# Optimization experiments

Measured on AMD Instinct MI355X. Metric: run time of the kernel, lower is better.

## Reference

```python
import jax, jax.numpy as jnp
import numpy as np

D_EMBED, D_K, D_V = 1024, 64, 64
B, S = 4, 4096


def setup_inputs() -> dict:
    key = jax.random.key(0)
    k1, k2, k3, k4 = jax.random.split(key, 4)
    x = jax.random.normal(k1, (B, S, D_EMBED), dtype=jnp.float32)
    # nn.Linear(d_embed, d) stores weight as [d, d_embed]
    Wq = jax.random.normal(k2, (D_K, D_EMBED), dtype=jnp.float32) * (D_EMBED ** -0.5)
    Wk = jax.random.normal(k3, (D_K, D_EMBED), dtype=jnp.float32) * (D_EMBED ** -0.5)
    Wv = jax.random.normal(k4, (D_V, D_EMBED), dtype=jnp.float32) * (D_EMBED ** -0.5)
    return {"x": x, "Wq": Wq, "Wk": Wk, "Wv": Wv}


def reference(x, Wq, Wk, Wv):
    # self-attention: y = z = x
    key = jnp.einsum('bse,ke->bsk', x, Wk)
    query = jnp.einsum('bse,ke->bsk', x, Wq)
    value = jnp.einsum('bse,ve->bsv', x, Wv)
    d_k = key.shape[-1]
    weight = jnp.einsum('bqk,bsk->bqs', query, key) / (d_k ** 0.5)
    # Faithful to torch: tril then masked_fill(weight == 0, -inf)
    weight = jnp.tril(weight)
    weight = jnp.where(weight == 0, -jnp.inf, weight)
    weight = jax.nn.softmax(weight, axis=-1)
    return jnp.einsum('bqs,bsv->bqv', weight, value)
```

## Files before the change

### kernel.cpp

```cpp
#include <hip/hip_runtime.h>
#include <hip/hip_bf16.h>


typedef short s16x8 __attribute__((ext_vector_type(8)));
typedef float f32x4 __attribute__((ext_vector_type(4)));
typedef float f32x16 __attribute__((ext_vector_type(16)));
typedef unsigned u32x2 __attribute__((ext_vector_type(2)));

#define MFMA16(a, b, c) __builtin_amdgcn_mfma_f32_16x16x32_bf16(a, b, c, 0, 0, 0)
#define MFMA32(a, b, c) __builtin_amdgcn_mfma_f32_32x32x16_bf16(a, b, c, 0, 0, 0)

constexpr int SEQ = 4096;
constexpr int DE  = 1024;

__device__ __forceinline__ short f2bf(float f) {
    union { float f; unsigned u; } v; v.f = f;
    unsigned r = (v.u + 0x7FFFu + ((v.u >> 16) & 1u)) >> 16;
    return (short)r;
}
__device__ __forceinline__ unsigned fbits(float f) { union { float f; unsigned u; } v; v.f = f; return v.u; }
__device__ __forceinline__ float bitsf(unsigned u) { union { unsigned u; float f; } v; v.u = u; return v.f; }
__device__ __forceinline__ unsigned pk2(float a, float b) {
    return (fbits(b) & 0xFFFF0000u) | (fbits(a) >> 16);
}

#define GLDS(gp, lp)                                                          \
    __builtin_amdgcn_global_load_lds(                                         \
        (const __attribute__((address_space(1))) unsigned int*)(gp),          \
        (__attribute__((address_space(3))) unsigned int*)(lp), 16, 0, 0)

__global__ __launch_bounds__(256) void k_convw(const float* __restrict__ Wq,
                                               const float* __restrict__ Wk,
                                               const float* __restrict__ Wv,
                                               short* __restrict__ Wb) {
    int i = (blockIdx.x * 256 + threadIdx.x) * 4;
    if (i >= 192 * 1024) return;
    int n = i >> 10, k = i & 1023;
    const float* src; float sc;
    if (n < 64)       { src = Wq + n * 1024;         sc = 0.18033688011112042f; }
    else if (n < 128) { src = Wk + (n - 64) * 1024;  sc = 1.0f; }
    else              { src = Wv + (n - 128) * 1024; sc = 1.0f; }
    float4 v = *(const float4*)(src + k);
    short4 o;
    o.x = f2bf(v.x * sc); o.y = f2bf(v.y * sc);
    o.z = f2bf(v.z * sc); o.w = f2bf(v.w * sc);
    *(short4*)(Wb + i) = o;
}

__global__ __launch_bounds__(512) void k_proj(const float* __restrict__ x,
                                              const short* __restrict__ Wb,
                                              short* __restrict__ Qs,
                                              short* __restrict__ Ks,
                                              short* __restrict__ Vt) {
    __shared__ __align__(16) char lds[2][40960];
    const int tid  = threadIdx.x;
    const int lane = tid & 63;
    const int c = lane & 15, g = (lane >> 4) & 3;
    const int wv = tid >> 6;
    const int rg = wv & 3, nh = wv >> 2;
    const int n0 = nh * 96;
    const int m0 = blockIdx.x * 64;

    const int Ar  = tid >> 4;
    const int Acs = ((tid & 15) << 4) ^ ((Ar & 7) << 4);
    const char* aS0 = (const char*)x + (((size_t)(m0 + Ar)) << 12) + Acs;
    const char* aS1 = aS0 + ((size_t)32 << 12);
    const int Wr  = tid >> 3;
    const int Wcs = ((tid & 7) << 4) ^ ((Wr & 7) << 4);
    const char* wS0 = (const char*)Wb + (((size_t)Wr) << 11) + Wcs;
    const char* wS1 = wS0 + ((size_t)64 << 11);
    const char* wS2 = wS0 + ((size_t)128 << 11);

    char* db0 = &lds[0][0] + tid * 16;
    char* db1 = &lds[1][0] + tid * 16;

    const int arow = rg * 16 + c;
    const int swz  = (c & 7) << 4;
    const char* aR[2] = { &lds[0][0] + arow * 256, &lds[1][0] + arow * 256 };
    const char* wR[2][6];
#pragma unroll
    for (int nf = 0; nf < 6; nf++) {
        int wrow = n0 + nf * 16 + c;
        wR[0][nf] = &lds[0][0] + 16384 + wrow * 128;
        wR[1][nf] = &lds[1][0] + 16384 + wrow * 128;
    }

    f32x4 acc[6];
#pragma unroll
    for (int i = 0; i < 6; i++) acc[i] = (f32x4){0.f, 0.f, 0.f, 0.f};

#define PSTAGE(kk, db) {                                  \
        GLDS(aS0 + (kk) * 256, (db));                     \
        GLDS(aS1 + (kk) * 256, (db) + 8192);              \
        GLDS(wS0 + (kk) * 128, (db) + 16384);             \
        GLDS(wS1 + (kk) * 128, (db) + 24576);             \
        GLDS(wS2 + (kk) * 128, (db) + 32768); }

#define PCOMPUTE(bi) {                                                         \
        _Pragma("unroll")                                                      \
        for (int kc = 0; kc < 2; kc++) {                                       \
            float4 a0 = *(const float4*)(aR[bi] + ((kc*128 + g*32)      ^ swz)); \
            float4 a1 = *(const float4*)(aR[bi] + ((kc*128 + g*32 + 16) ^ swz)); \
            s16x8 a;                                                           \
            a[0]=f2bf(a0.x); a[1]=f2bf(a0.y); a[2]=f2bf(a0.z); a[3]=f2bf(a0.w); \
            a[4]=f2bf(a1.x); a[5]=f2bf(a1.y); a[6]=f2bf(a1.z); a[7]=f2bf(a1.w); \
            _Pragma("unroll")                                                  \
            for (int nf = 0; nf < 6; nf++) {                                   \
                s16x8 bfr = *(const s16x8*)(wR[bi][nf] + ((kc*64 + g*16) ^ swz)); \
                acc[nf] = MFMA16(a, bfr, acc[nf]);                             \
            }                                                                  \
        } }

    PSTAGE(0, db0);
    PSTAGE(1, db1);

    for (int kk = 0; kk < 15; kk++) {
        asm volatile("s_waitcnt vmcnt(5)" ::: "memory");
        __builtin_amdgcn_sched_barrier(0);
        __builtin_amdgcn_s_barrier();
        if (kk & 1) PCOMPUTE(1) else PCOMPUTE(0)
        asm volatile("s_waitcnt lgkmcnt(0)" ::: "memory");
        __builtin_amdgcn_sched_barrier(0);
        __builtin_amdgcn_s_barrier();
        if (kk < 14) { if (kk & 1) PSTAGE(kk + 2, db1) else PSTAGE(kk + 2, db0) }
    }
    asm volatile("s_waitcnt vmcnt(0)" ::: "memory");
    __builtin_amdgcn_sched_barrier(0);
    __builtin_amdgcn_s_barrier();
    PCOMPUTE(1)
#undef PSTAGE
#undef PCOMPUTE

#pragma unroll
    for (int nf = 0; nf < 6; nf++) {
        int col16 = n0 + nf * 16;
        if (col16 < 64) {
            int col = col16 + c;
#pragma unroll
            for (int r = 0; r < 4; r++)
                Qs[(size_t)(m0 + rg * 16 + g * 4 + r) * 64 + col] = f2bf(acc[nf][r]);
        } else if (col16 < 128) {
            int col = col16 - 64 + c;
#pragma unroll
            for (int r = 0; r < 4; r++)
                Ks[(size_t)(m0 + rg * 16 + g * 4 + r) * 64 + col] = f2bf(acc[nf][r]);
        } else {
            int d  = col16 - 128 + c;
            int mm = m0 + rg * 16 + g * 4;
            int bt = mm >> 12, s0 = mm & (SEQ - 1);
            short4 o;
            o.x = f2bf(acc[nf][0]); o.y = f2bf(acc[nf][1]);
            o.z = f2bf(acc[nf][2]); o.w = f2bf(acc[nf][3]);
            *(short4*)(Vt + ((size_t)(bt * 64 + d)) * SEQ + s0) = o;
        }
    }
}

__global__ __launch_bounds__(256, 3) void k_attn(const short* __restrict__ Qs,
                                                 const short* __restrict__ Ks,
                                                 const short* __restrict__ Vt,
                                                 float* __restrict__ pws) {
    __shared__ __align__(16) char smem[2][16384];

    int tid = threadIdx.x;
    int l = tid & 63, wv = tid >> 6;
    int q = l & 31, hi = l >> 5;

    int ub = blockIdx.x >> 2, bt = blockIdx.x & 3;
    int u = ub, j = 31, cs = 8;
    while (u >= cs) { u -= cs; --j; cs = (j + 4) >> 2; }
    int seg = u;
    int kb0 = seg << 9;
    int kend_t = min(j * 128 + 128, kb0 + 512);
    const int R = (kend_t - kb0 + 63) >> 6;
    int q0 = j * 128 + wv * 32;
    int mycend = q0 + 32;

    const short* Qb = Qs + (size_t)bt * SEQ * 64;
    const short* Kb = Ks + (size_t)bt * SEQ * 64;
    const short* Vb = Vt + (size_t)bt * 64 * SEQ;

    s16x8 qf[4];
#pragma unroll
    for (int d = 0; d < 4; d++)
        qf[d] = *(const s16x8*)(Qb + (size_t)(q0 + q) * 64 + d * 16 + hi * 8);

    const int row8 = l >> 3;
    const int scs  = (l & 7) ^ row8;

#define ASTAGE(kb, b) {                                                        \
        _Pragma("unroll")                                                      \
        for (int i = 0; i < 2; i++) {                                          \
            GLDS(Kb + (((size_t)((kb) + wv*16 + i*8 + row8)) << 6) + scs*8,    \
                 &smem[b][0] + (wv*16 + i*8)*128);                             \
            GLDS(Vb + (size_t)(wv*16 + i*8 + row8) * SEQ + (kb) + scs*8,       \
                 &smem[b][0] + 8192 + (wv*16 + i*8)*128); } }

    f32x16 o0 = {}, o1 = {};
    float m = -1e30f, ll = 0.f;
    const int qs7 = q & 7;

    ASTAGE(kb0, 0);
    if (R > 1) ASTAGE(kb0 + 64, 1);

    for (int r = 0; r < R; r++) {
        if (r == R - 1) asm volatile("s_waitcnt vmcnt(0)" ::: "memory");
        else            asm volatile("s_waitcnt vmcnt(4)" ::: "memory");
        __builtin_amdgcn_sched_barrier(0);
        __builtin_amdgcn_s_barrier();
        __builtin_amdgcn_sched_barrier(0);

        int k0 = kb0 + r * 64;
        if (k0 < mycend) {
            const char* kl = &smem[r & 1][0];
            f32x16 sa = {}, sb = {};
#pragma unroll
            for (int dd = 0; dd < 4; dd++) {
                int ch = ((2 * dd + hi) ^ qs7) << 4;
                s16x8 ka = *(const s16x8*)(kl + q * 128 + ch);
                s16x8 kb2 = *(const s16x8*)(kl + (32 + q) * 128 + ch);
                sa = MFMA32(ka,  qf[dd], sa);
                sb = MFMA32(kb2, qf[dd], sb);
            }
            if (k0 + 31 > q0) {
#pragma unroll
                for (int rr = 0; rr < 16; rr++) {
                    int kv = k0 + (rr & 3) + 8 * (rr >> 2) + 4 * hi;
                    if (kv > q0 + q) sa[rr] = -3.0e38f;
                }
            }
            if (k0 + 63 > q0) {
#pragma unroll
                for (int rr = 0; rr < 16; rr++) {
                    int kv = k0 + 32 + (rr & 3) + 8 * (rr >> 2) + 4 * hi;
                    if (kv > q0 + q) sb[rr] = -3.0e38f;
                }
            }
            float t0 = -3.0e38f, t1 = -3.0e38f;
#pragma unroll
            for (int rr = 0; rr < 16; rr++) { t0 = fmaxf(t0, sa[rr]); t1 = fmaxf(t1, sb[rr]); }
            float tm = fmaxf(t0, t1);
            u32x2 sw = __builtin_amdgcn_permlane32_swap(fbits(tm), fbits(tm), false, false);
            tm = fmaxf(bitsf(sw[0]), bitsf(sw[1]));
            float mn = fmaxf(m, tm);
            float scale = __builtin_amdgcn_exp2f(m - mn);
            m = mn;
            float ss = 0.f;
#pragma unroll
            for (int rr = 0; rr < 16; rr++) {
                sa[rr] = __builtin_amdgcn_exp2f(sa[rr] - mn);
                sb[rr] = __builtin_amdgcn_exp2f(sb[rr] - mn);
                ss += sa[rr] + sb[rr];
            }
            sw = __builtin_amdgcn_permlane32_swap(fbits(ss), fbits(ss), false, false);
            ss = bitsf(sw[0]) + bitsf(sw[1]);
            ll = ll * scale + ss;
            o0 *= scale; o1 *= scale;

            union { unsigned u[4]; s16x8 v; } pA0, pA1, pB0, pB1;
            {
                unsigned A0 = pk2(sa[0], sa[1]),   B0 = pk2(sa[2], sa[3]);
                unsigned A1 = pk2(sa[4], sa[5]),   B1 = pk2(sa[6], sa[7]);
                unsigned A2 = pk2(sa[8], sa[9]),   B2 = pk2(sa[10], sa[11]);
                unsigned A3 = pk2(sa[12], sa[13]), B3 = pk2(sa[14], sa[15]);
                u32x2 r0 = __builtin_amdgcn_permlane32_swap(A0, A1, false, false);
                u32x2 r1 = __builtin_amdgcn_permlane32_swap(B0, B1, false, false);
                u32x2 r2 = __builtin_amdgcn_permlane32_swap(A2, A3, false, false);
                u32x2 r3 = __builtin_amdgcn_permlane32_swap(B2, B3, false, false);
                pA0.u[0] = r0[0]; pA0.u[1] = r1[0]; pA0.u[2] = r0[1]; pA0.u[3] = r1[1];
                pA1.u[0] = r2[0]; pA1.u[1] = r3[0]; pA1.u[2] = r2[1]; pA1.u[3] = r3[1];
            }
            {
                unsigned A0 = pk2(sb[0], sb[1]),   B0 = pk2(sb[2], sb[3]);
                unsigned A1 = pk2(sb[4], sb[5]),   B1 = pk2(sb[6], sb[7]);
                unsigned A2 = pk2(sb[8], sb[9]),   B2 = pk2(sb[10], sb[11]);
                unsigned A3 = pk2(sb[12], sb[13]), B3 = pk2(sb[14], sb[15]);
                u32x2 r0 = __builtin_amdgcn_permlane32_swap(A0, A1, false, false);
                u32x2 r1 = __builtin_amdgcn_permlane32_swap(B0, B1, false, false);
                u32x2 r2 = __builtin_amdgcn_permlane32_swap(A2, A3, false, false);
                u32x2 r3 = __builtin_amdgcn_permlane32_swap(B2, B3, false, false);
                pB0.u[0] = r0[0]; pB0.u[1] = r1[0]; pB0.u[2] = r0[1]; pB0.u[3] = r1[1];
                pB1.u[0] = r2[0]; pB1.u[1] = r3[0]; pB1.u[2] = r2[1]; pB1.u[3] = r3[1];
            }

            const char* vl = &smem[r & 1][0] + 8192;
            const char* v0p = vl + q * 128;
            const char* v1p = vl + (32 + q) * 128;
            int c0 = ((0 + hi) ^ qs7) << 4, c1 = ((2 + hi) ^ qs7) << 4;
            int c2 = ((4 + hi) ^ qs7) << 4, c3 = ((6 + hi) ^ qs7) << 4;
            o0 = MFMA32(*(const s16x8*)(v0p + c0), pA0.v, o0);
            o0 = MFMA32(*(const s16x8*)(v0p + c1), pA1.v, o0);
            o0 = MFMA32(*(const s16x8*)(v0p + c2), pB0.v, o0);
            o0 = MFMA32(*(const s16x8*)(v0p + c3), pB1.v, o0);
            o1 = MFMA32(*(const s16x8*)(v1p + c0), pA0.v, o1);
            o1 = MFMA32(*(const s16x8*)(v1p + c1), pA1.v, o1);
            o1 = MFMA32(*(const s16x8*)(v1p + c2), pB0.v, o1);
            o1 = MFMA32(*(const s16x8*)(v1p + c3), pB1.v, o1);
        }

        asm volatile("s_waitcnt lgkmcnt(0)" ::: "memory");
        __builtin_amdgcn_sched_barrier(0);
        __builtin_amdgcn_s_barrier();
        if (r + 2 < R) { if (r & 1) ASTAGE(kb0 + (r + 2) * 64, 1) else ASTAGE(kb0 + (r + 2) * 64, 0) }
    }
#undef ASTAGE

    float* p = pws + ((size_t)blockIdx.x * 4 + wv) * 2112;
#pragma unroll
    for (int rr = 0; rr < 16; rr++) {
        int dv = (rr & 3) + 8 * (rr >> 2) + 4 * hi;
        p[dv * 32 + q]        = o0[rr];
        p[(dv + 32) * 32 + q] = o1[rr];
    }
    if (hi == 0) { p[2048 + q] = m; p[2080 + q] = ll; }
}

__global__ __launch_bounds__(256) void k_comb(const float* __restrict__ pws,
                                              float* __restrict__ out) {
    int b = blockIdx.x;
    int bt = b & 3, j = (b >> 2) & 31, w = b >> 7;
    int nseg = (j + 4) >> 2;
    int ubb = 0;
    for (int jj = 31; jj > j; --jj) ubb += (jj + 4) >> 2;

    int tid = threadIdx.x;
    int q = tid >> 3, dv0 = (tid & 7) * 8;

    const float* rec[8];
    float ms[8];
    float M = -1e30f;
#pragma unroll
    for (int s = 0; s < 8; s++) {
        if (s < nseg) {
            rec[s] = pws + ((size_t)(((ubb + s) * 4 + bt) * 4 + w)) * 2112;
            ms[s] = rec[s][2048 + q];
            M = fmaxf(M, ms[s]);
        }
    }
    float L = 0.f, wsg[8];
#pragma unroll
    for (int s = 0; s < 8; s++) {
        if (s < nseg) {
            wsg[s] = __builtin_amdgcn_exp2f(ms[s] - M);
            L += wsg[s] * rec[s][2080 + q];
        }
    }
    float inv = 1.0f / L;
    float res[8];
#pragma unroll
    for (int i = 0; i < 8; i++) res[i] = 0.f;
#pragma unroll
    for (int s = 0; s < 8; s++) {
        if (s < nseg) {
#pragma unroll
            for (int i = 0; i < 8; i++)
                res[i] += wsg[s] * rec[s][(dv0 + i) * 32 + q];
        }
    }
    int qout = j * 128 + w * 32 + q;
    float* op = out + ((size_t)bt * SEQ + qout) * 64 + dv0;
    float4 f0 = {res[0] * inv, res[1] * inv, res[2] * inv, res[3] * inv};
    float4 f1 = {res[4] * inv, res[5] * inv, res[6] * inv, res[7] * inv};
    *(float4*)op = f0;
    *(float4*)(op + 4) = f1;
}

extern "C" void kernel_launch(void* const* d_in, const int* in_sizes, int n_in,
                              void* d_out, int out_size, void* d_ws, size_t ws_size,
                              hipStream_t stream) {
    const float* x  = (const float*)d_in[0];
    const float* Wq = (const float*)d_in[1];
    const float* Wk = (const float*)d_in[2];
    const float* Wv = (const float*)d_in[3];
    float* out = (float*)d_out;

    char* ws = (char*)d_ws;
    short* Wb = (short*)ws;
    short* Qs = (short*)(ws + 393216);
    short* Ks = (short*)(ws + 393216 + 2097152);
    short* Vt = (short*)(ws + 393216 + 2 * 2097152);
    float* pP = (float*)(ws + 6684672);

    k_convw<<<dim3(192), dim3(256), 0, stream>>>(Wq, Wk, Wv, Wb);
    k_proj <<<dim3(256), dim3(512), 0, stream>>>(x, Wb, Qs, Ks, Vt);
    k_attn <<<dim3(576), dim3(256), 0, stream>>>(Qs, Ks, Vt, pP);
    k_comb <<<dim3(512), dim3(256), 0, stream>>>(pP, out);
}
```

Before: 67.56 us.

## Process two query tiles per wave to reuse staged K/V fragments

Each attention wave now handles two 32-row query tiles (128 rows apart) against the same staged K/V block. K and V fragments are loaded into registers once and shared across both tiles' MFMAs, halving the block count (288) and the K/V LDS/global traffic per query. The partial-result layout and the combine kernel are reindexed to match. Occupancy drops from 3 to 2 blocks per CU because register pressure roughly doubles, and the smaller grid may leave CUs underused.

```diff
diff --git a/kernel.cpp b/kernel.cpp
--- a/kernel.cpp
+++ b/kernel.cpp
@@ -6,6 +6,7 @@
 typedef float f32x4 __attribute__((ext_vector_type(4)));
 typedef float f32x16 __attribute__((ext_vector_type(16)));
 typedef unsigned u32x2 __attribute__((ext_vector_type(2)));
+typedef union { unsigned u[4]; s16x8 v; } pfrag;
 
 #define MFMA16(a, b, c) __builtin_amdgcn_mfma_f32_16x16x32_bf16(a, b, c, 0, 0, 0)
 #define MFMA32(a, b, c) __builtin_amdgcn_mfma_f32_32x32x16_bf16(a, b, c, 0, 0, 0)
@@ -156,7 +157,96 @@
     }
 }
 
-__global__ __launch_bounds__(256, 3) void k_attn(const short* __restrict__ Qs,
+#define SMTREE(sa, sb, m, ll, o0, o1) {                                        \
+    float mx8[8];                                                              \
+    _Pragma("unroll")                                                          \
+    for (int i2 = 0; i2 < 8; i2++)                                             \
+        mx8[i2] = fmaxf(fmaxf(sa[i2], sa[i2 + 8]), fmaxf(sb[i2], sb[i2 + 8])); \
+    float tm_ = fmaxf(fmaxf(fmaxf(mx8[0], mx8[1]), fmaxf(mx8[2], mx8[3])),     \
+                      fmaxf(fmaxf(mx8[4], mx8[5]), fmaxf(mx8[6], mx8[7])));    \
+    u32x2 sw_ = __builtin_amdgcn_permlane32_swap(fbits(tm_), fbits(tm_), false, false); \
+    tm_ = fmaxf(bitsf(sw_[0]), bitsf(sw_[1]));                                 \
+    float mn_ = fmaxf(m, tm_);                                                 \
+    float sc_ = __builtin_amdgcn_exp2f(m - mn_);                               \
+    m = mn_;                                                                   \
+    _Pragma("unroll")                                                          \
+    for (int i2 = 0; i2 < 16; i2++) {                                          \
+        sa[i2] = __builtin_amdgcn_exp2f(sa[i2] - mn_);                         \
+        sb[i2] = __builtin_amdgcn_exp2f(sb[i2] - mn_);                         \
+    }                                                                          \
+    float s8_[8];                                                              \
+    _Pragma("unroll")                                                          \
+    for (int i2 = 0; i2 < 8; i2++)                                             \
+        s8_[i2] = (sa[i2] + sa[i2 + 8]) + (sb[i2] + sb[i2 + 8]);               \
+    float ss_ = ((s8_[0] + s8_[1]) + (s8_[2] + s8_[3]))                        \
+              + ((s8_[4] + s8_[5]) + (s8_[6] + s8_[7]));                       \
+    sw_ = __builtin_amdgcn_permlane32_swap(fbits(ss_), fbits(ss_), false, false); \
+    ss_ = bitsf(sw_[0]) + bitsf(sw_[1]);                                       \
+    ll = ll * sc_ + ss_;                                                       \
+    o0 *= sc_; o1 *= sc_; }
+
+#define PACKPH(sa, sb, u0, u1, u2, u3) {                                       \
+    unsigned A0 = pk2(sa[0], sa[1]),   B0 = pk2(sa[2], sa[3]);                 \
+    unsigned A1 = pk2(sa[4], sa[5]),   B1 = pk2(sa[6], sa[7]);                 \
+    unsigned A2 = pk2(sa[8], sa[9]),   B2 = pk2(sa[10], sa[11]);               \
+    unsigned A3 = pk2(sa[12], sa[13]), B3 = pk2(sa[14], sa[15]);               \
+    u32x2 r0_ = __builtin_amdgcn_permlane32_swap(A0, A1, false, false);        \
+    u32x2 r1_ = __builtin_amdgcn_permlane32_swap(B0, B1, false, false);        \
+    u32x2 r2_ = __builtin_amdgcn_permlane32_swap(A2, A3, false, false);        \
+    u32x2 r3_ = __builtin_amdgcn_permlane32_swap(B2, B3, false, false);        \
+    u0.u[0] = r0_[0]; u0.u[1] = r1_[0]; u0.u[2] = r0_[1]; u0.u[3] = r1_[1];    \
+    u1.u[0] = r2_[0]; u1.u[1] = r3_[0]; u1.u[2] = r2_[1]; u1.u[3] = r3_[1];    \
+    A0 = pk2(sb[0], sb[1]);   B0 = pk2(sb[2], sb[3]);                          \
+    A1 = pk2(sb[4], sb[5]);   B1 = pk2(sb[6], sb[7]);                          \
+    A2 = pk2(sb[8], sb[9]);   B2 = pk2(sb[10], sb[11]);                        \
+    A3 = pk2(sb[12], sb[13]); B3 = pk2(sb[14], sb[15]);                        \
+    r0_ = __builtin_amdgcn_permlane32_swap(A0, A1, false, false);              \
+    r1_ = __builtin_amdgcn_permlane32_swap(B0, B1, false, false);              \
+    r2_ = __builtin_amdgcn_permlane32_swap(A2, A3, false, false);              \
+    r3_ = __builtin_amdgcn_permlane32_swap(B2, B3, false, false);              \
+    u2.u[0] = r0_[0]; u2.u[1] = r1_[0]; u2.u[2] = r0_[1]; u2.u[3] = r1_[1];    \
+    u3.u[0] = r2_[0]; u3.u[1] = r3_[0]; u3.u[2] = r2_[1]; u3.u[3] = r3_[1]; }
+
+#define PROCT(qf, q0t, endt, m, ll, o0, o1) {                                  \
+    if (k0 < (endt)) {                                                         \
+        f32x16 sa = {}, sb = {};                                               \
+        _Pragma("unroll")                                                      \
+        for (int dd = 0; dd < 4; dd++) {                                       \
+            int ch = ((2 * dd + hi) ^ qs7) << 4;                               \
+            s16x8 ka  = *(const s16x8*)(kl + q * 128 + ch);                    \
+            s16x8 kb2 = *(const s16x8*)(kl + (32 + q) * 128 + ch);             \
+            sa = MFMA32(ka,  qf[dd], sa);                                      \
+            sb = MFMA32(kb2, qf[dd], sb);                                      \
+        }                                                                      \
+        if (k0 + 31 > (q0t)) {                                                 \
+            _Pragma("unroll")                                                  \
+            for (int rr = 0; rr < 16; rr++) {                                  \
+                int kv = k0 + (rr & 3) + 8 * (rr >> 2) + 4 * hi;               \
+                if (kv > (q0t) + q) sa[rr] = -3.0e38f;                         \
+            }                                                                  \
+        }                                                                      \
+        if (k0 + 63 > (q0t)) {                                                 \
+            _Pragma("unroll")                                                  \
+            for (int rr = 0; rr < 16; rr++) {                                  \
+                int kv = k0 + 32 + (rr & 3) + 8 * (rr >> 2) + 4 * hi;          \
+                if (kv > (q0t) + q) sb[rr] = -3.0e38f;                         \
+            }                                                                  \
+        }                                                                      \
+        SMTREE(sa, sb, m, ll, o0, o1);                                         \
+        pfrag u0_, u1_, u2_, u3_;                                              \
+        PACKPH(sa, sb, u0_, u1_, u2_, u3_);                                    \
+        _Pragma("unroll")                                                      \
+        for (int dd = 0; dd < 4; dd++) {                                       \
+            int ch = ((2 * dd + hi) ^ qs7) << 4;                               \
+            s16x8 va  = *(const s16x8*)(vl + q * 128 + ch);                    \
+            s16x8 vb2 = *(const s16x8*)(vl + (32 + q) * 128 + ch);             \
+            pfrag* uu = dd == 0 ? &u0_ : dd == 1 ? &u1_ : dd == 2 ? &u2_ : &u3_; \
+            o0 = MFMA32(va,  uu->v, o0);                                       \
+            o1 = MFMA32(vb2, uu->v, o1);                                       \
+        }                                                                      \
+    } }
+
+__global__ __launch_bounds__(256, 2) void k_attn(const short* __restrict__ Qs,
                                                  const short* __restrict__ Ks,
                                                  const short* __restrict__ Vt,
                                                  float* __restrict__ pws) {
@@ -167,23 +257,26 @@
     int q = l & 31, hi = l >> 5;
 
     int ub = blockIdx.x >> 2, bt = blockIdx.x & 3;
-    int u = ub, j = 31, cs = 8;
-    while (u >= cs) { u -= cs; --j; cs = (j + 4) >> 2; }
+    int u = ub, J = 15, cs = 8;
+    while (u >= cs) { u -= cs; --J; cs = (J + 2) >> 1; }
     int seg = u;
     int kb0 = seg << 9;
-    int kend_t = min(j * 128 + 128, kb0 + 512);
-    const int R = (kend_t - kb0 + 63) >> 6;
-    int q0 = j * 128 + wv * 32;
-    int mycend = q0 + 32;
+    int kend_t = min(J * 256 + 256, kb0 + 512);
+    const int R = (kend_t - kb0) >> 6;
+    const int q0A = J * 256 + wv * 32;
+    const int q0B = q0A + 128;
+    const int endA = q0A + 32, endB = q0B + 32;
 
     const short* Qb = Qs + (size_t)bt * SEQ * 64;
     const short* Kb = Ks + (size_t)bt * SEQ * 64;
     const short* Vb = Vt + (size_t)bt * 64 * SEQ;
 
-    s16x8 qf[4];
-#pragma unroll
-    for (int d = 0; d < 4; d++)
-        qf[d] = *(const s16x8*)(Qb + (size_t)(q0 + q) * 64 + d * 16 + hi * 8);
+    s16x8 qfA[4], qfB[4];
+#pragma unroll
+    for (int d = 0; d < 4; d++) {
+        qfA[d] = *(const s16x8*)(Qb + (size_t)(q0A + q) * 64 + d * 16 + hi * 8);
+        qfB[d] = *(const s16x8*)(Qb + (size_t)(q0B + q) * 64 + d * 16 + hi * 8);
+    }
 
     const int row8 = l >> 3;
     const int scs  = (l & 7) ^ row8;
@@ -196,8 +289,8 @@
             GLDS(Vb + (size_t)(wv*16 + i*8 + row8) * SEQ + (kb) + scs*8,       \
                  &smem[b][0] + 8192 + (wv*16 + i*8)*128); } }
 
-    f32x16 o0 = {}, o1 = {};
-    float m = -1e30f, ll = 0.f;
+    f32x16 oA0 = {}, oA1 = {}, oB0 = {}, oB1 = {};
+    float mA = -1e30f, llA = 0.f, mB = -1e30f, llB = 0.f;
     const int qs7 = q & 7;
 
     ASTAGE(kb0, 0);
@@ -211,91 +304,57 @@
         __builtin_amdgcn_sched_barrier(0);
 
         int k0 = kb0 + r * 64;
-        if (k0 < mycend) {
-            const char* kl = &smem[r & 1][0];
-            f32x16 sa = {}, sb = {};
+        const char* kl = &smem[r & 1][0];
+        const char* vl = kl + 8192;
+
+        if (k0 + 63 <= q0A) {
+            s16x8 kf[8];
 #pragma unroll
             for (int dd = 0; dd < 4; dd++) {
                 int ch = ((2 * dd + hi) ^ qs7) << 4;
-                s16x8 ka = *(const s16x8*)(kl + q * 128 + ch);
-                s16x8 kb2 = *(const s16x8*)(kl + (32 + q) * 128 + ch);
-                sa = MFMA32(ka,  qf[dd], sa);
-                sb = MFMA32(kb2, qf[dd], sb);
+                kf[dd]     = *(const s16x8*)(kl + q * 128 + ch);
+                kf[4 + dd] = *(const s16x8*)(kl + (32 + q) * 128 + ch);
             }
-            if (k0 + 31 > q0) {
-#pragma unroll
-                for (int rr = 0; rr < 16; rr++) {
-                    int kv = k0 + (rr & 3) + 8 * (rr >> 2) + 4 * hi;
-                    if (kv > q0 + q) sa[rr] = -3.0e38f;
-                }
+            f32x16 saA = {}, sbA = {}, saB = {}, sbB = {};
+#pragma unroll
+            for (int dd = 0; dd < 4; dd++) {
+                saA = MFMA32(kf[dd],     qfA[dd], saA);
+                sbA = MFMA32(kf[4 + dd], qfA[dd], sbA);
+                saB = MFMA32(kf[dd],     qfB[dd], saB);
+                sbB = MFMA32(kf[4 + dd], qfB[dd], sbB);
             }
-            if (k0 + 63 > q0) {
-#pragma unroll
-                for (int rr = 0; rr < 16; rr++) {
-                    int kv = k0 + 32 + (rr & 3) + 8 * (rr >> 2) + 4 * hi;
-                    if (kv > q0 + q) sb[rr] = -3.0e38f;
-                }
+            SMTREE(saA, sbA, mA, llA, oA0, oA1);
+            pfrag uA0, uA1, uA2, uA3;
+            PACKPH(saA, sbA, uA0, uA1, uA2, uA3);
+            s16x8 vf[8];
+#pragma unroll
+            for (int dd = 0; dd < 4; dd++) {
+                int ch = ((2 * dd + hi) ^ qs7) << 4;
+                vf[dd]     = *(const s16x8*)(vl + q * 128 + ch);
+                vf[4 + dd] = *(const s16x8*)(vl + (32 + q) * 128 + ch);
             }
-            float t0 = -3.0e38f, t1 = -3.0e38f;
-#pragma unroll
-            for (int rr = 0; rr < 16; rr++) { t0 = fmaxf(t0, sa[rr]); t1 = fmaxf(t1, sb[rr]); }
-            float tm = fmaxf(t0, t1);
-            u32x2 sw = __builtin_amdgcn_permlane32_swap(fbits(tm), fbits(tm), false, false);
-            tm = fmaxf(bitsf(sw[0]), bitsf(sw[1]));
-            float mn = fmaxf(m, tm);
-            float scale = __builtin_amdgcn_exp2f(m - mn);
-            m = mn;
-            float ss = 0.f;
-#pragma unroll
-            for (int rr = 0; rr < 16; rr++) {
-                sa[rr] = __builtin_amdgcn_exp2f(sa[rr] - mn);
-                sb[rr] = __builtin_amdgcn_exp2f(sb[rr] - mn);
-                ss += sa[rr] + sb[rr];
-            }
-            sw = __builtin_amdgcn_permlane32_swap(fbits(ss), fbits(ss), false, false);
-            ss = bitsf(sw[0]) + bitsf(sw[1]);
-            ll = ll * scale + ss;
-            o0 *= scale; o1 *= scale;
-
-            union { unsigned u[4]; s16x8 v; } pA0, pA1, pB0, pB1;
-            {
-                unsigned A0 = pk2(sa[0], sa[1]),   B0 = pk2(sa[2], sa[3]);
-                unsigned A1 = pk2(sa[4], sa[5]),   B1 = pk2(sa[6], sa[7]);
-                unsigned A2 = pk2(sa[8], sa[9]),   B2 = pk2(sa[10], sa[11]);
-                unsigned A3 = pk2(sa[12], sa[13]), B3 = pk2(sa[14], sa[15]);
-                u32x2 r0 = __builtin_amdgcn_permlane32_swap(A0, A1, false, false);
-                u32x2 r1 = __builtin_amdgcn_permlane32_swap(B0, B1, false, false);
-                u32x2 r2 = __builtin_amdgcn_permlane32_swap(A2, A3, false, false);
-                u32x2 r3 = __builtin_amdgcn_permlane32_swap(B2, B3, false, false);
-                pA0.u[0] = r0[0]; pA0.u[1] = r1[0]; pA0.u[2] = r0[1]; pA0.u[3] = r1[1];
-                pA1.u[0] = r2[0]; pA1.u[1] = r3[0]; pA1.u[2] = r2[1]; pA1.u[3] = r3[1];
-            }
-            {
-                unsigned A0 = pk2(sb[0], sb[1]),   B0 = pk2(sb[2], sb[3]);
-                unsigned A1 = pk2(sb[4], sb[5]),   B1 = pk2(sb[6], sb[7]);
-                unsigned A2 = pk2(sb[8], sb[9]),   B2 = pk2(sb[10], sb[11]);
-                unsigned A3 = pk2(sb[12], sb[13]), B3 = pk2(sb[14], sb[15]);
-                u32x2 r0 = __builtin_amdgcn_permlane32_swap(A0, A1, false, false);
-                u32x2 r1 = __builtin_amdgcn_permlane32_swap(B0, B1, false, false);
-                u32x2 r2 = __builtin_amdgcn_permlane32_swap(A2, A3, false, false);
-                u32x2 r3 = __builtin_amdgcn_permlane32_swap(B2, B3, false, false);
-                pB0.u[0] = r0[0]; pB0.u[1] = r1[0]; pB0.u[2] = r0[1]; pB0.u[3] = r1[1];
-                pB1.u[0] = r2[0]; pB1.u[1] = r3[0]; pB1.u[2] = r2[1]; pB1.u[3] = r3[1];
-            }
-
-            const char* vl = &smem[r & 1][0] + 8192;
-            const char* v0p = vl + q * 128;
-            const char* v1p = vl + (32 + q) * 128;
-            int c0 = ((0 + hi) ^ qs7) << 4, c1 = ((2 + hi) ^ qs7) << 4;
-            int c2 = ((4 + hi) ^ qs7) << 4, c3 = ((6 + hi) ^ qs7) << 4;
-            o0 = MFMA32(*(const s16x8*)(v0p + c0), pA0.v, o0);
-            o0 = MFMA32(*(const s16x8*)(v0p + c1), pA1.v, o0);
-            o0 = MFMA32(*(const s16x8*)(v0p + c2), pB0.v, o0);
-            o0 = MFMA32(*(const s16x8*)(v0p + c3), pB1.v, o0);
-            o1 = MFMA32(*(const s16x8*)(v1p + c0), pA0.v, o1);
-            o1 = MFMA32(*(const s16x8*)(v1p + c1), pA1.v, o1);
-            o1 = MFMA32(*(const s16x8*)(v1p + c2), pB0.v, o1);
-            o1 = MFMA32(*(const s16x8*)(v1p + c3), pB1.v, o1);
+            oA0 = MFMA32(vf[0], uA0.v, oA0);
+            oA0 = MFMA32(vf[1], uA1.v, oA0);
+            oA0 = MFMA32(vf[2], uA2.v, oA0);
+            oA0 = MFMA32(vf[3], uA3.v, oA0);
+            oA1 = MFMA32(vf[4], uA0.v, oA1);
+            oA1 = MFMA32(vf[5], uA1.v, oA1);
+            oA1 = MFMA32(vf[6], uA2.v, oA1);
+            oA1 = MFMA32(vf[7], uA3.v, oA1);
+            SMTREE(saB, sbB, mB, llB, oB0, oB1);
+            pfrag uB0, uB1, uB2, uB3;
+            PACKPH(saB, sbB, uB0, uB1, uB2, uB3);
+            oB0 = MFMA32(vf[0], uB0.v, oB0);
+            oB0 = MFMA32(vf[1], uB1.v, oB0);
+            oB0 = MFMA32(vf[2], uB2.v, oB0);
+            oB0 = MFMA32(vf[3], uB3.v, oB0);
+            oB1 = MFMA32(vf[4], uB0.v, oB1);
+            oB1 = MFMA32(vf[5], uB1.v, oB1);
+            oB1 = MFMA32(vf[6], uB2.v, oB1);
+            oB1 = MFMA32(vf[7], uB3.v, oB1);
+        } else {
+            PROCT(qfA, q0A, endA, mA, llA, oA0, oA1);
+            PROCT(qfB, q0B, endB, mB, llB, oB0, oB1);
         }
 
         asm volatile("s_waitcnt lgkmcnt(0)" ::: "memory");
@@ -305,44 +364,51 @@
     }
 #undef ASTAGE
 
-    float* p = pws + ((size_t)blockIdx.x * 4 + wv) * 2112;
-#pragma unroll
-    for (int rr = 0; rr < 16; rr++) {
-        int dv = (rr & 3) + 8 * (rr >> 2) + 4 * hi;
-        p[dv * 32 + q]        = o0[rr];
-        p[(dv + 32) * 32 + q] = o1[rr];
-    }
-    if (hi == 0) { p[2048 + q] = m; p[2080 + q] = ll; }
+    {
+        float* p = pws + ((size_t)(((bt * 16 + J) * 8 + wv) * 8 + seg)) * 2112;
+#pragma unroll
+        for (int rr = 0; rr < 16; rr++) {
+            int dv = (rr & 3) + 8 * (rr >> 2) + 4 * hi;
+            p[dv * 32 + q]        = oA0[rr];
+            p[(dv + 32) * 32 + q] = oA1[rr];
+        }
+        if (hi == 0) { p[2048 + q] = mA; p[2080 + q] = llA; }
+    }
+    {
+        float* p = pws + ((size_t)(((bt * 16 + J) * 8 + 4 + wv) * 8 + seg)) * 2112;
+#pragma unroll
+        for (int rr = 0; rr < 16; rr++) {
+            int dv = (rr & 3) + 8 * (rr >> 2) + 4 * hi;
+            p[dv * 32 + q]        = oB0[rr];
+            p[(dv + 32) * 32 + q] = oB1[rr];
+        }
+        if (hi == 0) { p[2048 + q] = mB; p[2080 + q] = llB; }
+    }
 }
 
 __global__ __launch_bounds__(256) void k_comb(const float* __restrict__ pws,
                                               float* __restrict__ out) {
     int b = blockIdx.x;
-    int bt = b & 3, j = (b >> 2) & 31, w = b >> 7;
-    int nseg = (j + 4) >> 2;
-    int ubb = 0;
-    for (int jj = 31; jj > j; --jj) ubb += (jj + 4) >> 2;
+    int sub = b & 7, J = (b >> 3) & 15, bt = b >> 7;
+    int qbase = J * 256 + (sub >> 2) * 128 + (sub & 3) * 32;
+    int nseg = (qbase + 32 + 511) >> 9;
 
     int tid = threadIdx.x;
     int q = tid >> 3, dv0 = (tid & 7) * 8;
-
-    const float* rec[8];
-    float ms[8];
+    const float* base = pws + (size_t)b * 8 * 2112;
+
+    float ms[8], wsg[8];
     float M = -1e30f;
 #pragma unroll
     for (int s = 0; s < 8; s++) {
-        if (s < nseg) {
-            rec[s] = pws + ((size_t)(((ubb + s) * 4 + bt) * 4 + w)) * 2112;
-            ms[s] = rec[s][2048 + q];
-            M = fmaxf(M, ms[s]);
-        }
-    }
-    float L = 0.f, wsg[8];
+        if (s < nseg) { ms[s] = base[s * 2112 + 2048 + q]; M = fmaxf(M, ms[s]); }
+    }
+    float L = 0.f;
 #pragma unroll
     for (int s = 0; s < 8; s++) {
         if (s < nseg) {
             wsg[s] = __builtin_amdgcn_exp2f(ms[s] - M);
-            L += wsg[s] * rec[s][2080 + q];
+            L += wsg[s] * base[s * 2112 + 2080 + q];
         }
     }
     float inv = 1.0f / L;
@@ -352,13 +418,12 @@
 #pragma unroll
     for (int s = 0; s < 8; s++) {
         if (s < nseg) {
-#pragma unroll
-            for (int i = 0; i < 8; i++)
-                res[i] += wsg[s] * rec[s][(dv0 + i) * 32 + q];
-        }
-    }
-    int qout = j * 128 + w * 32 + q;
-    float* op = out + ((size_t)bt * SEQ + qout) * 64 + dv0;
+            const float* po = base + s * 2112;
+#pragma unroll
+            for (int i = 0; i < 8; i++) res[i] += wsg[s] * po[(dv0 + i) * 32 + q];
+        }
+    }
+    float* op = out + ((size_t)bt * SEQ + qbase + q) * 64 + dv0;
     float4 f0 = {res[0] * inv, res[1] * inv, res[2] * inv, res[3] * inv};
     float4 f1 = {res[4] * inv, res[5] * inv, res[6] * inv, res[7] * inv};
     *(float4*)op = f0;
@@ -383,6 +448,6 @@
 
     k_convw<<<dim3(192), dim3(256), 0, stream>>>(Wq, Wk, Wv, Wb);
     k_proj <<<dim3(256), dim3(512), 0, stream>>>(x, Wb, Qs, Ks, Vt);
-    k_attn <<<dim3(576), dim3(256), 0, stream>>>(Qs, Ks, Vt, pP);
+    k_attn <<<dim3(288), dim3(256), 0, stream>>>(Qs, Ks, Vt, pP);
     k_comb <<<dim3(512), dim3(256), 0, stream>>>(pP, out);
 }
```

New measurement: 71.73 us. 1.06x slower.
